# Performance work log

Hardware: AMD Instinct MI355X
Metric: run time of the kernel (lower is better)

Reference implementation:

```python
import jax, jax.numpy as jnp
import numpy as np

B, T, CNN, HW = 512, 256, 512, 7
V, H = 37, 8  # vocab_size, hidden_size


def setup_inputs() -> dict:
    key = jax.random.key(0)
    ks = jax.random.split(key, 10)
    s = 0.1
    return {
        "features": jax.random.normal(ks[0], (B, CNN, HW, HW), jnp.float32),
        "captions": jax.random.normal(ks[1], (B, T, V), jnp.float32),
        "W_in": jax.random.normal(ks[2], (V, CNN), jnp.float32) * s,
        "b_in": jax.random.normal(ks[3], (V,), jnp.float32) * s,
        "W_ih": jax.random.normal(ks[4], (4 * H, V), jnp.float32) * s,
        "W_hh": jax.random.normal(ks[5], (4 * H, H), jnp.float32) * s,
        "b_ih": jax.random.normal(ks[6], (4 * H,), jnp.float32) * s,
        "b_hh": jax.random.normal(ks[7], (4 * H,), jnp.float32) * s,
        "W_out": jax.random.normal(ks[8], (V, H), jnp.float32) * s,
        "b_out": jax.random.normal(ks[9], (V,), jnp.float32) * s,
    }


def reference(features, captions, W_in, b_in, W_ih, W_hh, b_ih, b_hh, W_out, b_out):
    # AdaptiveAvgPool2d(1) + flatten + fc_in -> [B, V]
    feat = features.mean(axis=(2, 3)) @ W_in.T + b_in
    # input at t=0 is feat, at t>0 is captions[:, t-1]; build [T, B, V] sequence
    xs = jnp.concatenate([feat[None], jnp.swapaxes(captions, 0, 1)[:-1]], axis=0)

    def step(carry, x):
        h, c = carry
        gates = x @ W_ih.T + b_ih + h @ W_hh.T + b_hh  # [B, 4H]
        i, f, g, o = jnp.split(gates, 4, axis=1)  # PyTorch LSTMCell gate order
        i = jax.nn.sigmoid(i)
        f = jax.nn.sigmoid(f)
        g = jnp.tanh(g)
        o = jax.nn.sigmoid(o)
        c = f * c + i * g
        h = o * jnp.tanh(c)
        out = jax.nn.softmax(h @ W_out.T + b_out, axis=1)  # [B, V]
        return (h, c), out

    h0 = jnp.zeros((feat.shape[0], W_hh.shape[1]), feat.dtype)
    c0 = jnp.zeros_like(h0)
    _, outs = jax.lax.scan(step, (h0, c0), xs)  # outs: [T, B, V]
    return jnp.swapaxes(outs, 0, 1)  # [B, T, V]
```

## Files before the change

### kernel.cpp

```cpp
#include <hip/hip_runtime.h>
#include <math.h>

#define BB   512
#define TT   256
#define CNNC 512
#define VV   37
#define HH   8
#define G4   32
#define CH   16
#define NCH  (TT / CH)

#define L2E 1.4426950408889634f

typedef float f4_t __attribute__((ext_vector_type(4)));
typedef float f2_t __attribute__((ext_vector_type(2)));

template <int CTRL>
__device__ __forceinline__ float dpp_f(float x) {
    int r = __builtin_amdgcn_update_dpp(0, __float_as_int(x), CTRL, 0xF, 0xF, true);
    return __int_as_float(r);
}

__device__ __forceinline__ float rcp_f(float x) { return __builtin_amdgcn_rcpf(x); }
__device__ __forceinline__ float exp2_f(float x) { return __builtin_amdgcn_exp2f(x); }

__device__ __forceinline__ f2_t fma2(f2_t a, f2_t b, f2_t c) {
    return __builtin_elementwise_fma(a, b, c);
}
__device__ __forceinline__ f2_t sp2(float x) { f2_t v = {x, x}; return v; }

__global__ __launch_bounds__(256) void k_feat(const float* __restrict__ features,
                                              const float* __restrict__ W_in,
                                              const float* __restrict__ b_in,
                                              float* __restrict__ featp) {
    __shared__ __align__(16) float raw[128 * 49];
    __shared__ float pooled[128];
    const int b = blockIdx.x, qt = blockIdx.y, tid = threadIdx.x;
    const f4_t* src =
        (const f4_t*)(features + (size_t)b * CNNC * 49 + qt * (128 * 49));
    f4_t* dst = (f4_t*)raw;
    for (int i = tid; i < 128 * 49 / 4; i += 256)
        dst[i] = __builtin_nontemporal_load(&src[i]);
    __syncthreads();
    if (tid < 128) {
        const float* p = raw + tid * 49;
        float s = 0.f;
        #pragma unroll
        for (int i = 0; i < 49; ++i) s += p[i];
        pooled[tid] = s;
    }
    __syncthreads();
    const int v = tid >> 2, pp = tid & 3;
    if (v < VV) {
        const float* w = W_in + v * CNNC + qt * 128 + pp * 32;
        const float* q = pooled + pp * 32;
        float s = 0.f;
        #pragma unroll
        for (int i = 0; i < 32; ++i) s += q[i] * w[i];
        s += __shfl_xor(s, 1);
        s += __shfl_xor(s, 2);
        if (pp == 0)
            featp[(qt * BB + b) * VV + v] =
                s * (1.f / 49.f) + (qt == 0 ? b_in[v] : 0.f);
    }
}

#define TSTR 12
#define SSTR (CH * TSTR + 4)
#define RSTR 132
#define RING_T (CH * RSTR)

#define BAR() do {                                                          \
    asm volatile("s_waitcnt lgkmcnt(0)" ::: "memory");                      \
    __builtin_amdgcn_s_barrier();                                           \
    __builtin_amdgcn_sched_barrier(0);                                      \
} while (0)

#define STEP(p2) do {                                                       \
    const float ha0 = h;                                                    \
    const float ha1 = dpp_f<0x4E>(h);                                       \
    const float ha3 = dpp_f<0x141>(h);                                      \
    const float ha2 = dpp_f<0x4E>(ha3);                                     \
    const float ha7 = dpp_f<0x140>(h);                                      \
    const float ha4 = dpp_f<0x141>(ha7);                                    \
    const float ha5 = dpp_f<0x4E>(ha4);                                     \
    const float ha6 = dpp_f<0x1B>(ha7);                                     \
    f2_t acc0 = fma2(w2[0], sp2(ha0), p2);                                  \
    acc0 = fma2(w2[1], sp2(ha1), acc0);                                     \
    acc0 = fma2(w2[2], sp2(ha2), acc0);                                     \
    acc0 = fma2(w2[3], sp2(ha3), acc0);                                     \
    f2_t acc1 = w2[4] * sp2(ha4);                                           \
    acc1 = fma2(w2[5], sp2(ha5), acc1);                                     \
    acc1 = fma2(w2[6], sp2(ha6), acc1);                                     \
    acc1 = fma2(w2[7], sp2(ha7), acc1);                                     \
    const f2_t np2 = acc0 + acc1;                                           \
    const float eA = rcp_f(1.f + exp2_f(np2.x));       \
    const float uB = rcp_f(1.f + exp2_f(np2.y));   \
    const float gg = fmaf(-4.f * L2E, uB, 2.f * L2E);    \
    const float myU = r ? eA : eA * gg;           \
    const float otU = dpp_f<0xB1>(myU);                                     \
    const float fg  = r ? myU : otU;                                        \
    const float igg = r ? otU : myU;                                        \
    const float ogx = dpp_f<0xB1>(uB);                                      \
    const float og  = r ? uB : ogx;                                         \
    c = fmaf(fg, c, igg);                         \
    const float rv = rcp_f(1.f + exp2_f(c));                                \
    h = fmaf(og + og, rv, -og);                             \
} while (0)

#define SCHUNK(it) do {                                                     \
    const float* base = &ring[((it) % 3) * RING_T] + roff2w;                \
    f2_t pbuf[CH];                                                          \
    _Pragma("unroll")                                                       \
    for (int tl = 0; tl < CH; ++tl)                                         \
        pbuf[tl] = *(const f2_t*)&base[tl * RSTR];                          \
    float hsv[CH];                                                          \
    _Pragma("unroll")                                                       \
    for (int tl = 0; tl < CH; ++tl) {                                       \
        STEP(pbuf[tl]);                                                     \
        hsv[tl] = h;                                                        \
    }                                                                       \
    if (r == 0) {                                                           \
        float* hb = &hst[(((it) & 1) * 4 + s4) * SSTR + j];                 \
        _Pragma("unroll")                                                   \
        for (int i = 0; i < CH; ++i) hb[i * TSTR] = hsv[i];                 \
    }                                                                       \
} while (0)

#define PRODUCE_BODY(pk)                                                    \
    float acc[8];                                                           \
    _Pragma("unroll")                                                       \
    for (int g = 0; g < 8; ++g) acc[g] = bs[g];                             \
    _Pragma("unroll")                                                       \
    for (int v = 0; v < VV; ++v) {                                          \
        const float xv = xr[v];                                             \
        _Pragma("unroll")                                                   \
        for (int g = 0; g < 8; ++g) acc[g] += xv * Wih[(g0 + g) * VV + v];  \
    }                                                                       \
    float* dst = &ring[((pk) % 3) * RING_T + ptl * RSTR];                   \
    _Pragma("unroll")                                                       \
    for (int g = 0; g < 8; ++g) {                                           \
        const int gg = g0 + g;                                              \
        const float sc = (gg >= 16 && gg < 24) ? (-2.f * L2E) : (-L2E);     \
        dst[((gg & 15) * 4 + ps) * 2 + (gg >> 4)] = acc[g] * sc;            \
    }

#define PRODUCE(pk) do {                    \
    const int t = (pk) * CH + ptl;                                          \
    const float* x = captions + ((size_t)pb * TT + (t - 1)) * VV;           \
    float xr[VV];                                                           \
    _Pragma("unroll")                                                       \
    for (int v = 0; v < VV; ++v) xr[v] = x[v];                              \
    PRODUCE_BODY(pk)                                                        \
} while (0)

#define EMIT(pk) do {                                                       \
    const int os = lane >> 4, otl = lane & 15;                              \
    const float* hp = &hst[(((pk) & 1) * 4 + os) * SSTR + otl * TSTR];      \
    const f4_t h0 = *(const f4_t*)hp;                                       \
    const f4_t h1 = *(const f4_t*)(hp + 4);                                 \
    const f4_t* W4 = (const f4_t*)Wo;                                       \
    float z[VV];                                                            \
    float m = -1e30f;                                                       \
    _Pragma("unroll")                                                       \
    for (int v = 0; v < VV; ++v) {                                          \
        const f4_t w0 = W4[v * 2], w1 = W4[v * 2 + 1];                      \
        float sv = bo[v];                                                   \
        sv = fmaf(h0.x, w0.x, sv); sv = fmaf(h0.y, w0.y, sv);               \
        sv = fmaf(h0.z, w0.z, sv); sv = fmaf(h0.w, w0.w, sv);               \
        sv = fmaf(h1.x, w1.x, sv); sv = fmaf(h1.y, w1.y, sv);               \
        sv = fmaf(h1.z, w1.z, sv); sv = fmaf(h1.w, w1.w, sv);               \
        z[v] = sv;                                                          \
        m = fmaxf(m, sv);                                                   \
    }                                                                       \
    float sum = 0.f;                                                        \
    _Pragma("unroll")                                                       \
    for (int v = 0; v < VV; ++v) {                                          \
        z[v] = exp2_f((z[v] - m) * L2E);                                    \
        sum += z[v];                                                        \
    }                                                                       \
    const float rs = rcp_f(sum);                                            \
    const int ob = bg * 4 + os;                                             \
    const int ot = (pk) * CH + otl;                                         \
    float* op = out + ((size_t)ob * TT + ot) * VV;                          \
    _Pragma("unroll")                                                       \
    for (int v = 0; v < VV; ++v) op[v] = z[v] * rs;                         \
} while (0)

__global__ __launch_bounds__(384) void k_lstm(const float* __restrict__ W_hh,
                                              const float* __restrict__ captions,
                                              const float* __restrict__ W_ih,
                                              const float* __restrict__ b_ih,
                                              const float* __restrict__ b_hh,
                                              const float* __restrict__ featp,
                                              const float* __restrict__ W_out,
                                              const float* __restrict__ b_out,
                                              float* __restrict__ out) {
    __shared__ __align__(16) float ring[3 * RING_T];
    __shared__ __align__(16) float hst[2 * 4 * SSTR];
    __shared__ __align__(16) float Wih[G4 * VV];
    __shared__ __align__(16) float Wo[VV * HH];
    __shared__ float bo[VV];

    const int tid  = threadIdx.x;
    const int wv   = tid >> 6;
    const int lane = tid & 63;
    const int bg   = blockIdx.x;

    const int s4 = lane >> 4;
    const int q  = lane & 15;
    const int j  = q >> 1;
    const int r  = q & 1;
    const int rowA   = r * 8 + j;
    const int roff2w = (rowA * 4 + s4) * 2;

    const int p   = tid - 128;
    const int ptl = (p >> 4) & 15;
    const int ps  = (p >> 2) & 3;
    const int pq  = p & 3;
    const int g0  = pq * 8;
    const int pb  = bg * 4 + ps;

    f2_t w2[HH];
    float bs[8];

    if (wv == 0) {
        const int rowB = 16 + rowA;
        const float scA = -L2E;
        const float scB = r ? -L2E : (-2.f * L2E);
        #pragma unroll
        for (int m = 0; m < HH; ++m) {
            f2_t wp = {scA * W_hh[rowA * HH + (j ^ m)],
                       scB * W_hh[rowB * HH + (j ^ m)]};
            w2[m] = wp;
        }
    } else if (wv == 1) {
        for (int i = lane; i < VV * HH; i += 64) Wo[i] = W_out[i];
        if (lane < VV) bo[lane] = b_out[lane];
    } else {
        for (int i = p; i < G4 * VV; i += 256) Wih[i] = W_ih[i];
        #pragma unroll
        for (int g = 0; g < 8; ++g) bs[g] = b_ih[g0 + g] + b_hh[g0 + g];
    }
    BAR();

    if (wv >= 2) {
        float xr[VV];
        if (ptl == 0) {
            #pragma unroll
            for (int v = 0; v < VV; ++v)
                xr[v] = featp[pb * VV + v] + featp[(BB + pb) * VV + v] +
                        featp[(2 * BB + pb) * VV + v] +
                        featp[(3 * BB + pb) * VV + v];
        } else {
            const float* x = captions + ((size_t)pb * TT + (ptl - 1)) * VV;
            #pragma unroll
            for (int v = 0; v < VV; ++v) xr[v] = x[v];
        }
        PRODUCE_BODY(0)
    }
    BAR();

    float h = 0.f, c = 0.f;

    for (int it = 0; it < NCH + 1; ++it) {
        if (wv == 0) {
            if (it < NCH) SCHUNK(it);
        } else if (wv == 1) {
            if (it >= 1) EMIT(it - 1);
        } else {
            if (it < NCH - 1) PRODUCE(it + 1);
        }
        BAR();
    }
}

extern "C" void kernel_launch(void* const* d_in, const int* in_sizes, int n_in,
                              void* d_out, int out_size, void* d_ws, size_t ws_size,
                              hipStream_t stream) {
    const float* features = (const float*)d_in[0];
    const float* captions = (const float*)d_in[1];
    const float* W_in     = (const float*)d_in[2];
    const float* b_in     = (const float*)d_in[3];
    const float* W_ih     = (const float*)d_in[4];
    const float* W_hh     = (const float*)d_in[5];
    const float* b_ih     = (const float*)d_in[6];
    const float* b_hh     = (const float*)d_in[7];
    const float* W_out    = (const float*)d_in[8];
    const float* b_out    = (const float*)d_in[9];
    float* out = (float*)d_out;

    float* featp = (float*)d_ws;

    k_feat<<<dim3(BB, 4), 256, 0, stream>>>(features, W_in, b_in, featp);
    k_lstm<<<128,         384, 0, stream>>>(W_hh, captions, W_ih, b_ih, b_hh,
                                            featp, W_out, b_out, out);
}
```

Before: 163.9 us.

## Prefetch next recurrence chunk into registers with two-deep ring buffer

The recurrent wave now loads chunk it+1's precomputed input gates from LDS into registers before it runs the serial steps of chunk it, so LDS load latency moves off the critical path. The ring shrinks from three buffers to two, and the loop is unrolled by two so buffer parity is fixed at compile time. Producer waves now work two chunks ahead, and an extra prologue barrier sets up the first prefetch. This costs more registers in the recurrent wave and a more complex schedule.

```diff
diff --git a/kernel.cpp b/kernel.cpp
--- a/kernel.cpp
+++ b/kernel.cpp
@@ -108,16 +108,18 @@
     h = fmaf(og + og, rv, -og);                             \
 } while (0)
 
-#define SCHUNK(it) do {                                                     \
-    const float* base = &ring[((it) % 3) * RING_T] + roff2w;                \
-    f2_t pbuf[CH];                                                          \
+#define PREF(dst, par) do {                                                 \
+    const float* base = &ring[(par) * RING_T] + roff2w;                     \
     _Pragma("unroll")                                                       \
     for (int tl = 0; tl < CH; ++tl)                                         \
-        pbuf[tl] = *(const f2_t*)&base[tl * RSTR];                          \
+        dst[tl] = *(const f2_t*)&base[tl * RSTR];                           \
+} while (0)
+
+#define SCHUNK(cur, it) do {                                                \
     float hsv[CH];                                                          \
     _Pragma("unroll")                                                       \
     for (int tl = 0; tl < CH; ++tl) {                                       \
-        STEP(pbuf[tl]);                                                     \
+        STEP(cur[tl]);                                                      \
         hsv[tl] = h;                                                        \
     }                                                                       \
     if (r == 0) {                                                           \
@@ -127,7 +129,7 @@
     }                                                                       \
 } while (0)
 
-#define PRODUCE_BODY(pk)                                                    \
+#define PRODUCE_BODY(par)                                                   \
     float acc[8];                                                           \
     _Pragma("unroll")                                                       \
     for (int g = 0; g < 8; ++g) acc[g] = bs[g];                             \
@@ -137,7 +139,7 @@
         _Pragma("unroll")                                                   \
         for (int g = 0; g < 8; ++g) acc[g] += xv * Wih[(g0 + g) * VV + v];  \
     }                                                                       \
-    float* dst = &ring[((pk) % 3) * RING_T + ptl * RSTR];                   \
+    float* dst = &ring[(par) * RING_T + ptl * RSTR];                        \
     _Pragma("unroll")                                                       \
     for (int g = 0; g < 8; ++g) {                                           \
         const int gg = g0 + g;                                              \
@@ -145,13 +147,13 @@
         dst[((gg & 15) * 4 + ps) * 2 + (gg >> 4)] = acc[g] * sc;            \
     }
 
-#define PRODUCE(pk) do {                    \
+#define PRODUCE(pk, par) do {               \
     const int t = (pk) * CH + ptl;                                          \
     const float* x = captions + ((size_t)pb * TT + (t - 1)) * VV;           \
     float xr[VV];                                                           \
     _Pragma("unroll")                                                       \
     for (int v = 0; v < VV; ++v) xr[v] = x[v];                              \
-    PRODUCE_BODY(pk)                                                        \
+    PRODUCE_BODY(par)                                                       \
 } while (0)
 
 #define EMIT(pk) do {                                                       \
@@ -196,7 +198,7 @@
                                               const float* __restrict__ W_out,
                                               const float* __restrict__ b_out,
                                               float* __restrict__ out) {
-    __shared__ __align__(16) float ring[3 * RING_T];
+    __shared__ __align__(16) float ring[2 * RING_T];
     __shared__ __align__(16) float hst[2 * 4 * SSTR];
     __shared__ __align__(16) float Wih[G4 * VV];
     __shared__ __align__(16) float Wo[VV * HH];
@@ -222,6 +224,7 @@
     const int pb  = bg * 4 + ps;
 
     f2_t w2[HH];
+    f2_t cA[CH], cB[CH];
     float bs[8];
 
     if (wv == 0) {
@@ -261,17 +264,48 @@
     }
     BAR();
 
+    if (wv == 0) {
+        PREF(cA, 0);
+    } else if (wv >= 2) {
+        PRODUCE(1, 1);
+    }
+    BAR();
+
     float h = 0.f, c = 0.f;
 
-    for (int it = 0; it < NCH + 1; ++it) {
-        if (wv == 0) {
-            if (it < NCH) SCHUNK(it);
-        } else if (wv == 1) {
-            if (it >= 1) EMIT(it - 1);
-        } else {
-            if (it < NCH - 1) PRODUCE(it + 1);
+    for (int ou = 0; ou < 9; ++ou) {
+        {
+            const int it = ou * 2;
+            if (wv == 0) {
+                if (it < NCH) {
+                    if (it + 1 < NCH) PREF(cB, 1);
+                    __builtin_amdgcn_sched_barrier(0);
+                    SCHUNK(cA, it);
+                }
+            } else if (wv == 1) {
+                if (it >= 1) EMIT(it - 1);
+            } else {
+                if (it + 2 < NCH) PRODUCE(it + 2, 0);
+            }
+            BAR();
         }
-        BAR();
+        {
+            const int it = ou * 2 + 1;
+            if (it <= NCH) {
+                if (wv == 0) {
+                    if (it < NCH) {
+                        PREF(cA, 0);
+                        __builtin_amdgcn_sched_barrier(0);
+                        SCHUNK(cB, it);
+                    }
+                } else if (wv == 1) {
+                    EMIT(it - 1);
+                } else {
+                    if (it + 2 < NCH) PRODUCE(it + 2, 1);
+                }
+                BAR();
+            }
+        }
     }
 }
 
```

New measurement: 163.9 us. About the same (-0.0%).
